# Kernel tuning notes

Measured on AMD Instinct MI355X. Metric: run time of the kernel, lower is better.

## Reference

```python
import jax, jax.numpy as jnp
import numpy as np

N_NODES = 100000
N_EDGES = 1600000
DIM = 128
N_LAYERS = 3
N_GRAPHS = 2048


def setup_inputs() -> dict:
    key = jax.random.key(0)
    ks = jax.random.split(key, 6)
    x = jax.random.normal(ks[0], (N_NODES, DIM), dtype=jnp.float32)
    edge_index = jax.random.randint(ks[1], (2, N_EDGES), 0, N_NODES, dtype=jnp.int64)
    batch = jnp.sort(jax.random.randint(ks[2], (N_NODES,), 0, N_GRAPHS, dtype=jnp.int64))
    scale = 1.0 / np.sqrt(DIM)
    W1 = jax.random.normal(ks[3], (N_LAYERS, DIM, DIM), dtype=jnp.float32) * scale
    b1 = jnp.zeros((N_LAYERS, DIM), dtype=jnp.float32)
    W2 = jax.random.normal(ks[4], (N_LAYERS, DIM, DIM), dtype=jnp.float32) * scale
    b2 = jnp.zeros((N_LAYERS, DIM), dtype=jnp.float32)
    return {"x": x, "edge_index": edge_index, "batch": batch,
            "W1": W1, "b1": b1, "W2": W2, "b2": b2}


def reference(x, edge_index, batch, W1, b1, W2, b2):
    src, dst = edge_index[0], edge_index[1]
    n = x.shape[0]
    n_layers = W1.shape[0]
    for l in range(n_layers):
        # GINConv (eps=0): h_i = MLP( sum_{j in N(i)} x_j + x_i )
        agg = jax.ops.segment_sum(x[src], dst, num_segments=n)  # [N, D]
        h = agg + x
        h = jnp.maximum(h @ W1[l] + b1[l], 0.0) @ W2[l] + b2[l]
        x = jnp.maximum(h, 0.0)  # outer self.act
    # global_mean_pool over graph ids
    sums = jax.ops.segment_sum(x, batch, num_segments=N_GRAPHS)  # [G, D]
    counts = jax.ops.segment_sum(jnp.ones((n,), x.dtype), batch, num_segments=N_GRAPHS)
    return sums / jnp.maximum(counts, 1.0)[:, None]
```

## Files before the change

kernel.cpp:

```cpp
#include <hip/hip_runtime.h>
#include <hip/hip_bf16.h>
#include <stdint.h>

#define N_NODES  100000
#define N_PAD    100032
#define N_EDGES  1600000
#define DIM      128
#define N_LAYERS 3
#define N_GRAPHS 2048

#define BSHIFT   8
#define NBUCKET  391
#define P1CHUNK  4096
#define P1GRID   391

typedef _Float16 f16;
typedef __attribute__((ext_vector_type(4))) _Float16 f16x4;
typedef __attribute__((ext_vector_type(8))) _Float16 f16x8;
typedef __attribute__((ext_vector_type(4))) float f32x4;

#define MFMA16(a, b, c) __builtin_amdgcn_mfma_f32_16x16x32_f16((a), (b), (c), 0, 0, 0)

#define OFF_OFFS  0u
#define OFF_BHT   400064u
#define OFF_BST   401664u
#define OFF_GCUR  403264u
#define OFF_BLKH  404864u
#define OFF_ESRC  1016448u
#define OFF_PAIR  7416448u
#define OFF_X16   13816448u
#define OFF_A16   39424640u
#define OFF_B16   65032832u
#define OFF_W1T   90641024u
#define OFF_W2T   90739328u


__global__ __launch_bounds__(256) void k_bhist(const int* __restrict__ dst,
                                               int* __restrict__ btot, int* __restrict__ blkh) {
    __shared__ int h[NBUCKET];
    int tid = threadIdx.x, b = blockIdx.x;
    for (int i = tid; i < NBUCKET; i += 256) h[i] = 0;
    __syncthreads();
    int base = b * P1CHUNK;
    int n = min(P1CHUNK, N_EDGES - base);
    for (int i = tid; i < n; i += 256)
        atomicAdd(&h[dst[base + i] >> BSHIFT], 1);
    __syncthreads();
    for (int i = tid; i < NBUCKET; i += 256) {
        blkh[b * NBUCKET + i] = h[i];
        atomicAdd(&btot[i], h[i]);
    }
}

__global__ __launch_bounds__(256) void k_bscan(const int* __restrict__ btot,
                                               int* __restrict__ bstart,
                                               int* __restrict__ gcursor,
                                               int* __restrict__ offs) {
    __shared__ int s[512];
    int t = threadIdx.x;
    s[t]       = (t < NBUCKET) ? btot[t] : 0;
    s[t + 256] = (t + 256 < NBUCKET) ? btot[t + 256] : 0;
    __syncthreads();
    for (int off = 1; off < 512; off <<= 1) {
        int a0 = (t >= off) ? s[t - off] : 0;
        int a1 = (t + 256 >= off) ? s[t + 256 - off] : 0;
        __syncthreads();
        s[t] += a0; s[t + 256] += a1;
        __syncthreads();
    }
    int e0 = (t == 0) ? 0 : s[t - 1];
    int e1 = s[t + 255];
    if (t < NBUCKET) { bstart[t] = e0; gcursor[t] = e0; }
    int idx = t + 256;
    if (idx <= NBUCKET) { bstart[idx] = e1; if (idx < NBUCKET) gcursor[idx] = e1; }
    if (t == 0) offs[N_NODES] = N_EDGES;
}

__global__ __launch_bounds__(256) void k_part1(const int* __restrict__ src, const int* __restrict__ dst,
                                               const int* __restrict__ blkh, int* __restrict__ gcursor,
                                               uint32_t* __restrict__ pairs) {
    __shared__ int gbase[NBUCKET];
    __shared__ int cur[NBUCKET];
    int tid = threadIdx.x, b = blockIdx.x;
    for (int i = tid; i < NBUCKET; i += 256) {
        int h = blkh[b * NBUCKET + i];
        gbase[i] = atomicAdd(&gcursor[i], h);
        cur[i] = 0;
    }
    __syncthreads();
    int base = b * P1CHUNK;
    int n = min(P1CHUNK, N_EDGES - base);
    for (int i = tid; i < n; i += 256) {
        int d = dst[base + i], s = src[base + i];
        int bin = d >> BSHIFT;
        int slot = atomicAdd(&cur[bin], 1);
        pairs[gbase[bin] + slot] = ((uint32_t)s << 8) | (uint32_t)(d & 255);
    }
}

__global__ __launch_bounds__(256) void k_part2(const uint32_t* __restrict__ pairs,
                                               const int* __restrict__ bstart,
                                               int* __restrict__ offs, int* __restrict__ esrc) {
    __shared__ int cnt[256];
    __shared__ int cur[256];
    __shared__ int sc[256];
    int t = threadIdx.x, b = blockIdx.x;
    int n0 = b << BSHIFT;
    int nn = min(256, N_NODES - n0);
    int e0 = bstart[b], e1 = bstart[b + 1];
    cnt[t] = 0;
    __syncthreads();
    for (int i = e0 + t; i < e1; i += 256)
        atomicAdd(&cnt[pairs[i] & 255], 1);
    __syncthreads();
    int my = cnt[t];
    sc[t] = my;
    __syncthreads();
    for (int off = 1; off < 256; off <<= 1) {
        int v = (t >= off) ? sc[t - off] : 0;
        __syncthreads();
        sc[t] += v;
        __syncthreads();
    }
    int excl = sc[t] - my;
    cur[t] = excl;
    if (t < nn) offs[n0 + t] = e0 + excl;
    __syncthreads();
    for (int i = e0 + t; i < e1; i += 256) {
        uint32_t p = pairs[i];
        int pos = e0 + atomicAdd(&cur[p & 255], 1);
        esrc[pos] = (int)(p >> 8);
    }
}


#define CVTX_BLOCKS 6250

__global__ void k_cvt(const float* __restrict__ x,
                      const float* __restrict__ W1, const float* __restrict__ W2,
                      f16* __restrict__ x16, f16* __restrict__ W1t, f16* __restrict__ W2t) {
    int b = blockIdx.x;
    if (b < CVTX_BLOCKS) {
        size_t i = ((size_t)b * 256 + threadIdx.x) * 8;
        float4 v0 = *(const float4*)&x[i];
        float4 v1 = *(const float4*)&x[i + 4];
        f16x8 h;
        h[0] = (f16)v0.x; h[1] = (f16)v0.y; h[2] = (f16)v0.z; h[3] = (f16)v0.w;
        h[4] = (f16)v1.x; h[5] = (f16)v1.y; h[6] = (f16)v1.z; h[7] = (f16)v1.w;
        *(f16x8*)&x16[i] = h;
    } else {
        int t = (b - CVTX_BLOCKS) * 256 + threadIdx.x;
        bool first = t < 49152;
        const float* W = first ? W1 : W2;
        f16* Wt = first ? W1t : W2t;
        int u = first ? t : t - 49152;
        int l = u >> 14;
        int kn = u & 16383;
        int k = kn >> 7, nn = kn & 127;
        Wt[l * 16384 + nn * 128 + k] = (f16)W[u];
    }
}


#define BM 64
#define LDS_K 136

template <bool POOL>
__global__ __launch_bounds__(512) void k_fused(
    const f16* __restrict__ xin, f16* __restrict__ xout,
    const int* __restrict__ offs, const int* __restrict__ esrc,
    const f16* __restrict__ W1t, const float* __restrict__ b1,
    const f16* __restrict__ W2t, const float* __restrict__ b2,
    const int* __restrict__ batch, float* __restrict__ gsum)
{
    __shared__ __align__(16) f16 tile[BM * LDS_K];
    __shared__ int sbatch[BM];
    int tid  = threadIdx.x;
    int lane = tid & 63;
    int w    = tid >> 6;
    int fr   = lane & 15;
    int fg   = lane >> 4;
    int row0 = blockIdx.x * BM;

    if (POOL && tid < BM) {
        int node = row0 + tid;
        sbatch[tid] = (node < N_NODES) ? batch[node] : -1;
    }

    {
        const f16x8* xr = (const f16x8*)xin;
        int c = fr;
#pragma unroll
        for (int b_ = 0; b_ < 2; b_++) {
            int r = w * 8 + b_ * 4 + fg;
            int node = row0 + r;
            f16x8 sum = {(f16)0, (f16)0, (f16)0, (f16)0, (f16)0, (f16)0, (f16)0, (f16)0};
            if (node < N_NODES) {
                sum = xr[(size_t)node * 16 + c];
                int e0 = offs[node], e1 = offs[node + 1];
                int e = e0;
                for (; e + 8 <= e1; e += 8) {
                    int s0 = esrc[e + 0], s1 = esrc[e + 1], s2 = esrc[e + 2], s3 = esrc[e + 3];
                    int s4 = esrc[e + 4], s5 = esrc[e + 5], s6 = esrc[e + 6], s7 = esrc[e + 7];
                    f16x8 v0 = xr[(size_t)s0 * 16 + c], v1 = xr[(size_t)s1 * 16 + c];
                    f16x8 v2 = xr[(size_t)s2 * 16 + c], v3 = xr[(size_t)s3 * 16 + c];
                    f16x8 v4 = xr[(size_t)s4 * 16 + c], v5 = xr[(size_t)s5 * 16 + c];
                    f16x8 v6 = xr[(size_t)s6 * 16 + c], v7 = xr[(size_t)s7 * 16 + c];
                    sum += (v0 + v1) + (v2 + v3);
                    sum += (v4 + v5) + (v6 + v7);
                }
                if (e < e1) {
                    int i1 = e + 1, i2 = e + 2, i3 = e + 3, i4 = e + 4, i5 = e + 5, i6 = e + 6, i7 = e + 7;
                    bool k1 = i1 < e1, k2 = i2 < e1, k3 = i3 < e1, k4 = i4 < e1,
                         k5 = i5 < e1, k6 = i6 < e1, k7 = i7 < e1;
                    int s0 = esrc[e];
                    int s1 = esrc[k1 ? i1 : e], s2 = esrc[k2 ? i2 : e], s3 = esrc[k3 ? i3 : e];
                    int s4 = esrc[k4 ? i4 : e], s5 = esrc[k5 ? i5 : e], s6 = esrc[k6 ? i6 : e];
                    int s7 = esrc[k7 ? i7 : e];
                    f16x8 v0 = xr[(size_t)s0 * 16 + c], v1 = xr[(size_t)s1 * 16 + c];
                    f16x8 v2 = xr[(size_t)s2 * 16 + c], v3 = xr[(size_t)s3 * 16 + c];
                    f16x8 v4 = xr[(size_t)s4 * 16 + c], v5 = xr[(size_t)s5 * 16 + c];
                    f16x8 v6 = xr[(size_t)s6 * 16 + c], v7 = xr[(size_t)s7 * 16 + c];
                    sum += v0;
                    if (k1) sum += v1;
                    if (k2) sum += v2;
                    if (k3) sum += v3;
                    if (k4) sum += v4;
                    if (k5) sum += v5;
                    if (k6) sum += v6;
                    if (k7) sum += v7;
                }
            }
            *(f16x8*)&tile[r * LDS_K + c * 8] = sum;
        }
    }

    int col = w * 16 + fr;
    f16x8 wf[4];
    float4 bv;
#pragma unroll
    for (int ks = 0; ks < 4; ks++)
        wf[ks] = *(const f16x8*)&W1t[col * DIM + ks * 32 + fg * 8];
    bv = *(const float4*)&b1[w * 16 + fg * 4];
    __syncthreads();

    f32x4 acc[4];
#pragma unroll
    for (int mt = 0; mt < 4; mt++) acc[mt] = (f32x4){0.f, 0.f, 0.f, 0.f};
#pragma unroll
    for (int mt = 0; mt < 4; mt++)
#pragma unroll
        for (int ks = 0; ks < 4; ks++) {
            f16x8 a = *(const f16x8*)&tile[(mt * 16 + fr) * LDS_K + ks * 32 + fg * 8];
            acc[mt] = MFMA16(wf[ks], a, acc[mt]);
        }
    __syncthreads();

#pragma unroll
    for (int mt = 0; mt < 4; mt++) {
        f16x4 hv;
        hv[0] = (f16)fmaxf(acc[mt][0] + bv.x, 0.f);
        hv[1] = (f16)fmaxf(acc[mt][1] + bv.y, 0.f);
        hv[2] = (f16)fmaxf(acc[mt][2] + bv.z, 0.f);
        hv[3] = (f16)fmaxf(acc[mt][3] + bv.w, 0.f);
        *(f16x4*)&tile[(mt * 16 + fr) * LDS_K + w * 16 + fg * 4] = hv;
    }

#pragma unroll
    for (int ks = 0; ks < 4; ks++)
        wf[ks] = *(const f16x8*)&W2t[col * DIM + ks * 32 + fg * 8];
    bv = *(const float4*)&b2[w * 16 + fg * 4];
    __syncthreads();

#pragma unroll
    for (int mt = 0; mt < 4; mt++) acc[mt] = (f32x4){0.f, 0.f, 0.f, 0.f};
#pragma unroll
    for (int mt = 0; mt < 4; mt++)
#pragma unroll
        for (int ks = 0; ks < 4; ks++) {
            f16x8 a = *(const f16x8*)&tile[(mt * 16 + fr) * LDS_K + ks * 32 + fg * 8];
            acc[mt] = MFMA16(wf[ks], a, acc[mt]);
        }

    if (!POOL) {
#pragma unroll
        for (int mt = 0; mt < 4; mt++) {
            f16x4 ov;
            ov[0] = (f16)fmaxf(acc[mt][0] + bv.x, 0.f);
            ov[1] = (f16)fmaxf(acc[mt][1] + bv.y, 0.f);
            ov[2] = (f16)fmaxf(acc[mt][2] + bv.z, 0.f);
            ov[3] = (f16)fmaxf(acc[mt][3] + bv.w, 0.f);
            *(f16x4*)&xout[(size_t)(row0 + mt * 16 + fr) * DIM + w * 16 + fg * 4] = ov;
        }
    } else {
        __syncthreads();
#pragma unroll
        for (int mt = 0; mt < 4; mt++) {
            f16x4 ov;
            ov[0] = (f16)fmaxf(acc[mt][0] + bv.x, 0.f);
            ov[1] = (f16)fmaxf(acc[mt][1] + bv.y, 0.f);
            ov[2] = (f16)fmaxf(acc[mt][2] + bv.z, 0.f);
            ov[3] = (f16)fmaxf(acc[mt][3] + bv.w, 0.f);
            *(f16x4*)&tile[(mt * 16 + fr) * LDS_K + w * 16 + fg * 4] = ov;
        }
        __syncthreads();

        int half = tid >> 7;
        int d = tid & 127;
        int rA = half * 16, rB = rA + 16;
        float s = 0.f;
        int curg = sbatch[rA];
        for (int r = rA; r < rB; r++) {
            int g = sbatch[r];
            if (g != curg) {
                if (curg >= 0) atomicAdd(&gsum[(size_t)curg * DIM + d], s);
                s = 0.f; curg = g;
            }
            if (g >= 0) s += (float)tile[r * LDS_K + d];
        }
        if (curg >= 0) atomicAdd(&gsum[(size_t)curg * DIM + d], s);
    }
}


__global__ void k_div(float* __restrict__ out, const int* __restrict__ batch) {
    int g = blockIdx.x;
    int d = threadIdx.x;
    int lo = 0, hi = N_NODES;
    while (lo < hi) { int m = (lo + hi) >> 1; if (batch[m] < g) lo = m + 1; else hi = m; }
    int start = lo;
    hi = N_NODES;
    while (lo < hi) { int m = (lo + hi) >> 1; if (batch[m] <= g) lo = m + 1; else hi = m; }
    int end = lo;
    float cntf = (float)(end - start);
    out[(size_t)g * DIM + d] /= fmaxf(cntf, 1.f);
}


extern "C" void kernel_launch(void* const* d_in, const int* in_sizes, int n_in,
                              void* d_out, int out_size, void* d_ws, size_t ws_size,
                              hipStream_t stream) {
    const float* x     = (const float*)d_in[0];
    const int*   ei    = (const int*)d_in[1];
    const int*   batch = (const int*)d_in[2];
    const float* W1    = (const float*)d_in[3];
    const float* b1    = (const float*)d_in[4];
    const float* W2    = (const float*)d_in[5];
    const float* b2    = (const float*)d_in[6];
    const int* srcp = ei;
    const int* dstp = ei + N_EDGES;

    char* ws = (char*)d_ws;
    int*      offs  = (int*)(ws + OFF_OFFS);
    int*      btot  = (int*)(ws + OFF_BHT);
    int*      bst   = (int*)(ws + OFF_BST);
    int*      gcur  = (int*)(ws + OFF_GCUR);
    int*      blkh  = (int*)(ws + OFF_BLKH);
    int*      esrc  = (int*)(ws + OFF_ESRC);
    uint32_t* pairs = (uint32_t*)(ws + OFF_PAIR);
    f16*      x16   = (f16*)(ws + OFF_X16);
    f16*      a16   = (f16*)(ws + OFF_A16);
    f16*      b16   = (f16*)(ws + OFF_B16);
    f16*      w1t   = (f16*)(ws + OFF_W1T);
    f16*      w2t   = (f16*)(ws + OFF_W2T);
    float*    outp  = (float*)d_out;

    hipMemsetAsync(btot, 0, NBUCKET * sizeof(int), stream);
    k_bhist<<<P1GRID, 256, 0, stream>>>(dstp, btot, blkh);
    k_bscan<<<1, 256, 0, stream>>>(btot, bst, gcur, offs);
    k_part1<<<P1GRID, 256, 0, stream>>>(srcp, dstp, blkh, gcur, pairs);
    k_part2<<<NBUCKET, 256, 0, stream>>>(pairs, bst, offs, esrc);

    k_cvt<<<CVTX_BLOCKS + 384, 256, 0, stream>>>(x, W1, W2, x16, w1t, w2t);

    hipMemsetAsync(outp, 0, (size_t)N_GRAPHS * DIM * sizeof(float), stream);

    k_fused<false><<<N_PAD / BM, 512, 0, stream>>>(x16, a16, offs, esrc,
                                                   w1t, b1, w2t, b2, batch, outp);
    k_fused<false><<<N_PAD / BM, 512, 0, stream>>>(a16, b16, offs, esrc,
                                                   w1t + 16384, b1 + DIM, w2t + 16384, b2 + DIM, batch, outp);
    k_fused<true><<<N_PAD / BM, 512, 0, stream>>>(b16, a16, offs, esrc,
                                                  w1t + 32768, b1 + 2 * DIM, w2t + 32768, b2 + 2 * DIM, batch, outp);

    k_div<<<N_GRAPHS, DIM, 0, stream>>>(outp, batch);
}
```

Measured before the change: 291.4 us.

## Merge preprocessing kernels, fold bucket scan into partition, halve fused row tile

Combines the x/W conversion, bucket histogram and output zeroing into one launch, and removes the standalone scan kernel by recomputing the bucket prefix sum inside each partition block. The gcursor array is now zeroed by the memset and used as a relative offset. The fused GIN layer kernel now handles 32 rows per block instead of 64, which doubles the block count and gives each wave one gather row. The aim is fewer launches and serial gaps, plus more parallelism in the gather. The cost is a redundant scan in every partition block and less reuse of the weights loaded per block.

```diff
diff --git a/kernel.cpp b/kernel.cpp
--- a/kernel.cpp
+++ b/kernel.cpp
@@ -23,133 +23,40 @@
 
 #define OFF_OFFS  0u
 #define OFF_BHT   400064u
-#define OFF_BST   401664u
-#define OFF_GCUR  403264u
-#define OFF_BLKH  404864u
-#define OFF_ESRC  1016448u
-#define OFF_PAIR  7416448u
-#define OFF_X16   13816448u
-#define OFF_A16   39424640u
-#define OFF_B16   65032832u
-#define OFF_W1T   90641024u
-#define OFF_W2T   90739328u
-
-
-__global__ __launch_bounds__(256) void k_bhist(const int* __restrict__ dst,
-                                               int* __restrict__ btot, int* __restrict__ blkh) {
+#define OFF_GCUR  401664u
+#define OFF_BLKH  403264u
+#define OFF_ESRC  1014848u
+#define OFF_PAIR  7414848u
+#define OFF_X16   13814848u
+#define OFF_A16   39423040u
+#define OFF_B16   65031232u
+#define OFF_W1T   90639424u
+#define OFF_W2T   90737728u
+
+
+#define CVTX_BLOCKS 6250
+#define CVTW_BLOCKS 384
+#define ZERO_BLOCKS 128
+#define PRE_GRID    (CVTX_BLOCKS + CVTW_BLOCKS + P1GRID + ZERO_BLOCKS)
+
+__global__ __launch_bounds__(256) void k_pre(
+    const float* __restrict__ x, const float* __restrict__ W1, const float* __restrict__ W2,
+    f16* __restrict__ x16, f16* __restrict__ W1t, f16* __restrict__ W2t,
+    const int* __restrict__ dst, int* __restrict__ btot, int* __restrict__ blkh,
+    float* __restrict__ outp)
+{
     __shared__ int h[NBUCKET];
-    int tid = threadIdx.x, b = blockIdx.x;
-    for (int i = tid; i < NBUCKET; i += 256) h[i] = 0;
-    __syncthreads();
-    int base = b * P1CHUNK;
-    int n = min(P1CHUNK, N_EDGES - base);
-    for (int i = tid; i < n; i += 256)
-        atomicAdd(&h[dst[base + i] >> BSHIFT], 1);
-    __syncthreads();
-    for (int i = tid; i < NBUCKET; i += 256) {
-        blkh[b * NBUCKET + i] = h[i];
-        atomicAdd(&btot[i], h[i]);
-    }
-}
-
-__global__ __launch_bounds__(256) void k_bscan(const int* __restrict__ btot,
-                                               int* __restrict__ bstart,
-                                               int* __restrict__ gcursor,
-                                               int* __restrict__ offs) {
-    __shared__ int s[512];
-    int t = threadIdx.x;
-    s[t]       = (t < NBUCKET) ? btot[t] : 0;
-    s[t + 256] = (t + 256 < NBUCKET) ? btot[t + 256] : 0;
-    __syncthreads();
-    for (int off = 1; off < 512; off <<= 1) {
-        int a0 = (t >= off) ? s[t - off] : 0;
-        int a1 = (t + 256 >= off) ? s[t + 256 - off] : 0;
-        __syncthreads();
-        s[t] += a0; s[t + 256] += a1;
-        __syncthreads();
-    }
-    int e0 = (t == 0) ? 0 : s[t - 1];
-    int e1 = s[t + 255];
-    if (t < NBUCKET) { bstart[t] = e0; gcursor[t] = e0; }
-    int idx = t + 256;
-    if (idx <= NBUCKET) { bstart[idx] = e1; if (idx < NBUCKET) gcursor[idx] = e1; }
-    if (t == 0) offs[N_NODES] = N_EDGES;
-}
-
-__global__ __launch_bounds__(256) void k_part1(const int* __restrict__ src, const int* __restrict__ dst,
-                                               const int* __restrict__ blkh, int* __restrict__ gcursor,
-                                               uint32_t* __restrict__ pairs) {
-    __shared__ int gbase[NBUCKET];
-    __shared__ int cur[NBUCKET];
-    int tid = threadIdx.x, b = blockIdx.x;
-    for (int i = tid; i < NBUCKET; i += 256) {
-        int h = blkh[b * NBUCKET + i];
-        gbase[i] = atomicAdd(&gcursor[i], h);
-        cur[i] = 0;
-    }
-    __syncthreads();
-    int base = b * P1CHUNK;
-    int n = min(P1CHUNK, N_EDGES - base);
-    for (int i = tid; i < n; i += 256) {
-        int d = dst[base + i], s = src[base + i];
-        int bin = d >> BSHIFT;
-        int slot = atomicAdd(&cur[bin], 1);
-        pairs[gbase[bin] + slot] = ((uint32_t)s << 8) | (uint32_t)(d & 255);
-    }
-}
-
-__global__ __launch_bounds__(256) void k_part2(const uint32_t* __restrict__ pairs,
-                                               const int* __restrict__ bstart,
-                                               int* __restrict__ offs, int* __restrict__ esrc) {
-    __shared__ int cnt[256];
-    __shared__ int cur[256];
-    __shared__ int sc[256];
-    int t = threadIdx.x, b = blockIdx.x;
-    int n0 = b << BSHIFT;
-    int nn = min(256, N_NODES - n0);
-    int e0 = bstart[b], e1 = bstart[b + 1];
-    cnt[t] = 0;
-    __syncthreads();
-    for (int i = e0 + t; i < e1; i += 256)
-        atomicAdd(&cnt[pairs[i] & 255], 1);
-    __syncthreads();
-    int my = cnt[t];
-    sc[t] = my;
-    __syncthreads();
-    for (int off = 1; off < 256; off <<= 1) {
-        int v = (t >= off) ? sc[t - off] : 0;
-        __syncthreads();
-        sc[t] += v;
-        __syncthreads();
-    }
-    int excl = sc[t] - my;
-    cur[t] = excl;
-    if (t < nn) offs[n0 + t] = e0 + excl;
-    __syncthreads();
-    for (int i = e0 + t; i < e1; i += 256) {
-        uint32_t p = pairs[i];
-        int pos = e0 + atomicAdd(&cur[p & 255], 1);
-        esrc[pos] = (int)(p >> 8);
-    }
-}
-
-
-#define CVTX_BLOCKS 6250
-
-__global__ void k_cvt(const float* __restrict__ x,
-                      const float* __restrict__ W1, const float* __restrict__ W2,
-                      f16* __restrict__ x16, f16* __restrict__ W1t, f16* __restrict__ W2t) {
-    int b = blockIdx.x;
+    int b = blockIdx.x, tid = threadIdx.x;
     if (b < CVTX_BLOCKS) {
-        size_t i = ((size_t)b * 256 + threadIdx.x) * 8;
+        size_t i = ((size_t)b * 256 + tid) * 8;
         float4 v0 = *(const float4*)&x[i];
         float4 v1 = *(const float4*)&x[i + 4];
-        f16x8 h;
-        h[0] = (f16)v0.x; h[1] = (f16)v0.y; h[2] = (f16)v0.z; h[3] = (f16)v0.w;
-        h[4] = (f16)v1.x; h[5] = (f16)v1.y; h[6] = (f16)v1.z; h[7] = (f16)v1.w;
-        *(f16x8*)&x16[i] = h;
-    } else {
-        int t = (b - CVTX_BLOCKS) * 256 + threadIdx.x;
+        f16x8 o;
+        o[0] = (f16)v0.x; o[1] = (f16)v0.y; o[2] = (f16)v0.z; o[3] = (f16)v0.w;
+        o[4] = (f16)v1.x; o[5] = (f16)v1.y; o[6] = (f16)v1.z; o[7] = (f16)v1.w;
+        *(f16x8*)&x16[i] = o;
+    } else if (b < CVTX_BLOCKS + CVTW_BLOCKS) {
+        int t = (b - CVTX_BLOCKS) * 256 + tid;
         bool first = t < 49152;
         const float* W = first ? W1 : W2;
         f16* Wt = first ? W1t : W2t;
@@ -158,11 +65,114 @@
         int kn = u & 16383;
         int k = kn >> 7, nn = kn & 127;
         Wt[l * 16384 + nn * 128 + k] = (f16)W[u];
-    }
-}
-
-
-#define BM 64
+    } else if (b < CVTX_BLOCKS + CVTW_BLOCKS + P1GRID) {
+        int bb = b - CVTX_BLOCKS - CVTW_BLOCKS;
+        for (int i = tid; i < NBUCKET; i += 256) h[i] = 0;
+        __syncthreads();
+        int base = bb * P1CHUNK;
+        int n = min(P1CHUNK, N_EDGES - base);
+        for (int i = tid; i < n; i += 256)
+            atomicAdd(&h[dst[base + i] >> BSHIFT], 1);
+        __syncthreads();
+        for (int i = tid; i < NBUCKET; i += 256) {
+            blkh[bb * NBUCKET + i] = h[i];
+            atomicAdd(&btot[i], h[i]);
+        }
+    } else {
+        int bb = b - CVTX_BLOCKS - CVTW_BLOCKS - P1GRID;
+        size_t i = ((size_t)bb * 256 + tid) * 8;
+        float4 z = {0.f, 0.f, 0.f, 0.f};
+        *(float4*)&outp[i] = z;
+        *(float4*)&outp[i + 4] = z;
+    }
+}
+
+
+__global__ __launch_bounds__(256) void k_part1(const int* __restrict__ src, const int* __restrict__ dst,
+                                               const int* __restrict__ blkh, const int* __restrict__ btot,
+                                               int* __restrict__ gcur, uint32_t* __restrict__ pairs) {
+    __shared__ int bs[512];
+    __shared__ int gbase[NBUCKET];
+    __shared__ int cur[NBUCKET];
+    int t = threadIdx.x, b = blockIdx.x;
+    bs[t]       = (t < NBUCKET) ? btot[t] : 0;
+    bs[t + 256] = (t + 256 < NBUCKET) ? btot[t + 256] : 0;
+    __syncthreads();
+    for (int off = 1; off < 512; off <<= 1) {
+        int a0 = (t >= off) ? bs[t - off] : 0;
+        int a1 = (t + 256 >= off) ? bs[t + 256 - off] : 0;
+        __syncthreads();
+        bs[t] += a0; bs[t + 256] += a1;
+        __syncthreads();
+    }
+    for (int i = t; i < NBUCKET; i += 256) {
+        int ex = (i == 0) ? 0 : bs[i - 1];
+        int h = blkh[b * NBUCKET + i];
+        gbase[i] = ex + atomicAdd(&gcur[i], h);
+        cur[i] = 0;
+    }
+    __syncthreads();
+    int base = b * P1CHUNK;
+    int n = min(P1CHUNK, N_EDGES - base);
+    for (int i = t; i < n; i += 256) {
+        int d = dst[base + i], s = src[base + i];
+        int bin = d >> BSHIFT;
+        int slot = atomicAdd(&cur[bin], 1);
+        pairs[gbase[bin] + slot] = ((uint32_t)s << 8) | (uint32_t)(d & 255);
+    }
+}
+
+
+__global__ __launch_bounds__(256) void k_part2(const uint32_t* __restrict__ pairs,
+                                               const int* __restrict__ btot,
+                                               int* __restrict__ offs, int* __restrict__ esrc) {
+    __shared__ int bs[512];
+    __shared__ int cnt[256];
+    __shared__ int cur[256];
+    __shared__ int sc[256];
+    int t = threadIdx.x, b = blockIdx.x;
+    bs[t]       = (t < NBUCKET) ? btot[t] : 0;
+    bs[t + 256] = (t + 256 < NBUCKET) ? btot[t + 256] : 0;
+    __syncthreads();
+    for (int off = 1; off < 512; off <<= 1) {
+        int a0 = (t >= off) ? bs[t - off] : 0;
+        int a1 = (t + 256 >= off) ? bs[t + 256 - off] : 0;
+        __syncthreads();
+        bs[t] += a0; bs[t + 256] += a1;
+        __syncthreads();
+    }
+    int e0 = (b == 0) ? 0 : bs[b - 1];
+    int e1 = bs[b];
+    if (b == 0 && t == 0) offs[N_NODES] = N_EDGES;
+    int n0 = b << BSHIFT;
+    int nn = min(256, N_NODES - n0);
+    cnt[t] = 0;
+    __syncthreads();
+    for (int i = e0 + t; i < e1; i += 256)
+        atomicAdd(&cnt[pairs[i] & 255], 1);
+    __syncthreads();
+    int my = cnt[t];
+    sc[t] = my;
+    __syncthreads();
+    for (int off = 1; off < 256; off <<= 1) {
+        int v = (t >= off) ? sc[t - off] : 0;
+        __syncthreads();
+        sc[t] += v;
+        __syncthreads();
+    }
+    int excl = sc[t] - my;
+    cur[t] = excl;
+    if (t < nn) offs[n0 + t] = e0 + excl;
+    __syncthreads();
+    for (int i = e0 + t; i < e1; i += 256) {
+        uint32_t p = pairs[i];
+        int pos = e0 + atomicAdd(&cur[p & 255], 1);
+        esrc[pos] = (int)(p >> 8);
+    }
+}
+
+
+#define BM 32
 #define LDS_K 136
 
 template <bool POOL>
@@ -190,49 +200,46 @@
     {
         const f16x8* xr = (const f16x8*)xin;
         int c = fr;
-#pragma unroll
-        for (int b_ = 0; b_ < 2; b_++) {
-            int r = w * 8 + b_ * 4 + fg;
-            int node = row0 + r;
-            f16x8 sum = {(f16)0, (f16)0, (f16)0, (f16)0, (f16)0, (f16)0, (f16)0, (f16)0};
-            if (node < N_NODES) {
-                sum = xr[(size_t)node * 16 + c];
-                int e0 = offs[node], e1 = offs[node + 1];
-                int e = e0;
-                for (; e + 8 <= e1; e += 8) {
-                    int s0 = esrc[e + 0], s1 = esrc[e + 1], s2 = esrc[e + 2], s3 = esrc[e + 3];
-                    int s4 = esrc[e + 4], s5 = esrc[e + 5], s6 = esrc[e + 6], s7 = esrc[e + 7];
-                    f16x8 v0 = xr[(size_t)s0 * 16 + c], v1 = xr[(size_t)s1 * 16 + c];
-                    f16x8 v2 = xr[(size_t)s2 * 16 + c], v3 = xr[(size_t)s3 * 16 + c];
-                    f16x8 v4 = xr[(size_t)s4 * 16 + c], v5 = xr[(size_t)s5 * 16 + c];
-                    f16x8 v6 = xr[(size_t)s6 * 16 + c], v7 = xr[(size_t)s7 * 16 + c];
-                    sum += (v0 + v1) + (v2 + v3);
-                    sum += (v4 + v5) + (v6 + v7);
-                }
-                if (e < e1) {
-                    int i1 = e + 1, i2 = e + 2, i3 = e + 3, i4 = e + 4, i5 = e + 5, i6 = e + 6, i7 = e + 7;
-                    bool k1 = i1 < e1, k2 = i2 < e1, k3 = i3 < e1, k4 = i4 < e1,
-                         k5 = i5 < e1, k6 = i6 < e1, k7 = i7 < e1;
-                    int s0 = esrc[e];
-                    int s1 = esrc[k1 ? i1 : e], s2 = esrc[k2 ? i2 : e], s3 = esrc[k3 ? i3 : e];
-                    int s4 = esrc[k4 ? i4 : e], s5 = esrc[k5 ? i5 : e], s6 = esrc[k6 ? i6 : e];
-                    int s7 = esrc[k7 ? i7 : e];
-                    f16x8 v0 = xr[(size_t)s0 * 16 + c], v1 = xr[(size_t)s1 * 16 + c];
-                    f16x8 v2 = xr[(size_t)s2 * 16 + c], v3 = xr[(size_t)s3 * 16 + c];
-                    f16x8 v4 = xr[(size_t)s4 * 16 + c], v5 = xr[(size_t)s5 * 16 + c];
-                    f16x8 v6 = xr[(size_t)s6 * 16 + c], v7 = xr[(size_t)s7 * 16 + c];
-                    sum += v0;
-                    if (k1) sum += v1;
-                    if (k2) sum += v2;
-                    if (k3) sum += v3;
-                    if (k4) sum += v4;
-                    if (k5) sum += v5;
-                    if (k6) sum += v6;
-                    if (k7) sum += v7;
-                }
+        int r = w * 4 + fg;
+        int node = row0 + r;
+        f16x8 sum = {(f16)0, (f16)0, (f16)0, (f16)0, (f16)0, (f16)0, (f16)0, (f16)0};
+        if (node < N_NODES) {
+            sum = xr[(size_t)node * 16 + c];
+            int e0 = offs[node], e1 = offs[node + 1];
+            int e = e0;
+            for (; e + 8 <= e1; e += 8) {
+                int s0 = esrc[e + 0], s1 = esrc[e + 1], s2 = esrc[e + 2], s3 = esrc[e + 3];
+                int s4 = esrc[e + 4], s5 = esrc[e + 5], s6 = esrc[e + 6], s7 = esrc[e + 7];
+                f16x8 v0 = xr[(size_t)s0 * 16 + c], v1 = xr[(size_t)s1 * 16 + c];
+                f16x8 v2 = xr[(size_t)s2 * 16 + c], v3 = xr[(size_t)s3 * 16 + c];
+                f16x8 v4 = xr[(size_t)s4 * 16 + c], v5 = xr[(size_t)s5 * 16 + c];
+                f16x8 v6 = xr[(size_t)s6 * 16 + c], v7 = xr[(size_t)s7 * 16 + c];
+                sum += (v0 + v1) + (v2 + v3);
+                sum += (v4 + v5) + (v6 + v7);
             }
-            *(f16x8*)&tile[r * LDS_K + c * 8] = sum;
-        }
+            if (e < e1) {
+                int i1 = e + 1, i2 = e + 2, i3 = e + 3, i4 = e + 4, i5 = e + 5, i6 = e + 6, i7 = e + 7;
+                bool k1 = i1 < e1, k2 = i2 < e1, k3 = i3 < e1, k4 = i4 < e1,
+                     k5 = i5 < e1, k6 = i6 < e1, k7 = i7 < e1;
+                int s0 = esrc[e];
+                int s1 = esrc[k1 ? i1 : e], s2 = esrc[k2 ? i2 : e], s3 = esrc[k3 ? i3 : e];
+                int s4 = esrc[k4 ? i4 : e], s5 = esrc[k5 ? i5 : e], s6 = esrc[k6 ? i6 : e];
+                int s7 = esrc[k7 ? i7 : e];
+                f16x8 v0 = xr[(size_t)s0 * 16 + c], v1 = xr[(size_t)s1 * 16 + c];
+                f16x8 v2 = xr[(size_t)s2 * 16 + c], v3 = xr[(size_t)s3 * 16 + c];
+                f16x8 v4 = xr[(size_t)s4 * 16 + c], v5 = xr[(size_t)s5 * 16 + c];
+                f16x8 v6 = xr[(size_t)s6 * 16 + c], v7 = xr[(size_t)s7 * 16 + c];
+                sum += v0;
+                if (k1) sum += v1;
+                if (k2) sum += v2;
+                if (k3) sum += v3;
+                if (k4) sum += v4;
+                if (k5) sum += v5;
+                if (k6) sum += v6;
+                if (k7) sum += v7;
+            }
+        }
+        *(f16x8*)&tile[r * LDS_K + c * 8] = sum;
     }
 
     int col = w * 16 + fr;
@@ -244,11 +251,11 @@
     bv = *(const float4*)&b1[w * 16 + fg * 4];
     __syncthreads();
 
-    f32x4 acc[4];
-#pragma unroll
-    for (int mt = 0; mt < 4; mt++) acc[mt] = (f32x4){0.f, 0.f, 0.f, 0.f};
-#pragma unroll
-    for (int mt = 0; mt < 4; mt++)
+    f32x4 acc[2];
+#pragma unroll
+    for (int mt = 0; mt < 2; mt++) acc[mt] = (f32x4){0.f, 0.f, 0.f, 0.f};
+#pragma unroll
+    for (int mt = 0; mt < 2; mt++)
 #pragma unroll
         for (int ks = 0; ks < 4; ks++) {
             f16x8 a = *(const f16x8*)&tile[(mt * 16 + fr) * LDS_K + ks * 32 + fg * 8];
@@ -257,7 +264,7 @@
     __syncthreads();
 
 #pragma unroll
-    for (int mt = 0; mt < 4; mt++) {
+    for (int mt = 0; mt < 2; mt++) {
         f16x4 hv;
         hv[0] = (f16)fmaxf(acc[mt][0] + bv.x, 0.f);
         hv[1] = (f16)fmaxf(acc[mt][1] + bv.y, 0.f);
@@ -273,9 +280,9 @@
     __syncthreads();
 
 #pragma unroll
-    for (int mt = 0; mt < 4; mt++) acc[mt] = (f32x4){0.f, 0.f, 0.f, 0.f};
-#pragma unroll
-    for (int mt = 0; mt < 4; mt++)
+    for (int mt = 0; mt < 2; mt++) acc[mt] = (f32x4){0.f, 0.f, 0.f, 0.f};
+#pragma unroll
+    for (int mt = 0; mt < 2; mt++)
 #pragma unroll
         for (int ks = 0; ks < 4; ks++) {
             f16x8 a = *(const f16x8*)&tile[(mt * 16 + fr) * LDS_K + ks * 32 + fg * 8];
@@ -284,7 +291,7 @@
 
     if (!POOL) {
 #pragma unroll
-        for (int mt = 0; mt < 4; mt++) {
+        for (int mt = 0; mt < 2; mt++) {
             f16x4 ov;
             ov[0] = (f16)fmaxf(acc[mt][0] + bv.x, 0.f);
             ov[1] = (f16)fmaxf(acc[mt][1] + bv.y, 0.f);
@@ -295,7 +302,7 @@
     } else {
         __syncthreads();
 #pragma unroll
-        for (int mt = 0; mt < 4; mt++) {
+        for (int mt = 0; mt < 2; mt++) {
             f16x4 ov;
             ov[0] = (f16)fmaxf(acc[mt][0] + bv.x, 0.f);
             ov[1] = (f16)fmaxf(acc[mt][1] + bv.y, 0.f);
@@ -307,7 +314,7 @@
 
         int half = tid >> 7;
         int d = tid & 127;
-        int rA = half * 16, rB = rA + 16;
+        int rA = half * 8, rB = rA + 8;
         float s = 0.f;
         int curg = sbatch[rA];
         for (int r = rA; r < rB; r++) {
@@ -353,7 +360,6 @@
     char* ws = (char*)d_ws;
     int*      offs  = (int*)(ws + OFF_OFFS);
     int*      btot  = (int*)(ws + OFF_BHT);
-    int*      bst   = (int*)(ws + OFF_BST);
     int*      gcur  = (int*)(ws + OFF_GCUR);
     int*      blkh  = (int*)(ws + OFF_BLKH);
     int*      esrc  = (int*)(ws + OFF_ESRC);
@@ -365,15 +371,11 @@
     f16*      w2t   = (f16*)(ws + OFF_W2T);
     float*    outp  = (float*)d_out;
 
-    hipMemsetAsync(btot, 0, NBUCKET * sizeof(int), stream);
-    k_bhist<<<P1GRID, 256, 0, stream>>>(dstp, btot, blkh);
-    k_bscan<<<1, 256, 0, stream>>>(btot, bst, gcur, offs);
-    k_part1<<<P1GRID, 256, 0, stream>>>(srcp, dstp, blkh, gcur, pairs);
-    k_part2<<<NBUCKET, 256, 0, stream>>>(pairs, bst, offs, esrc);
-
-    k_cvt<<<CVTX_BLOCKS + 384, 256, 0, stream>>>(x, W1, W2, x16, w1t, w2t);
-
-    hipMemsetAsync(outp, 0, (size_t)N_GRAPHS * DIM * sizeof(float), stream);
+    hipMemsetAsync(btot, 0, 3200, stream);
+    k_pre<<<PRE_GRID, 256, 0, stream>>>(x, W1, W2, x16, w1t, w2t, dstp, btot, blkh, outp);
+
+    k_part1<<<P1GRID, 256, 0, stream>>>(srcp, dstp, blkh, btot, gcur, pairs);
+    k_part2<<<NBUCKET, 256, 0, stream>>>(pairs, btot, offs, esrc);
 
     k_fused<false><<<N_PAD / BM, 512, 0, stream>>>(x16, a16, offs, esrc,
                                                    w1t, b1, w2t, b2, batch, outp);
```

After: 333.5 us. 1.14x slower.
